# Kernel optimization log

Measured on AMD Instinct MI355X. Metric: run time of the kernel, lower is better.

Reference implementation:

```python
import jax, jax.numpy as jnp
import numpy as np

# Model config (matches init_kwargs)
B, J, D_IN, D_MODEL, NUM_HEADS, NUM_LAYERS = 1024, 24, 64, 512, 8, 6
A = J + 1  # joints + cls token
LN_EPS = 1e-5


def setup_inputs() -> dict:
    key = jax.random.key(0)
    ks = jax.random.split(key, 14)
    s = 0.02  # weight init scale
    return {
        "x": jax.random.normal(ks[0], (B, J, D_IN), dtype=jnp.float32),
        # per-joint input embeddings: Linear(d_in, d_model) x J
        "We": jax.random.normal(ks[1], (J, D_IN, D_MODEL), dtype=jnp.float32) * s,
        "be": jnp.zeros((J, D_MODEL), dtype=jnp.float32),
        "cls_token": jax.random.normal(ks[2], (D_MODEL,), dtype=jnp.float32),
        # per-layer shared key/value projections
        "Wk": jax.random.normal(ks[3], (NUM_LAYERS, D_MODEL, D_MODEL), dtype=jnp.float32) * s,
        "bk": jnp.zeros((NUM_LAYERS, D_MODEL), dtype=jnp.float32),
        "Wv": jax.random.normal(ks[4], (NUM_LAYERS, D_MODEL, D_MODEL), dtype=jnp.float32) * s,
        "bv": jnp.zeros((NUM_LAYERS, D_MODEL), dtype=jnp.float32),
        # per-layer, PER-JOINT query projections (ModuleList of A linears)
        "Wq": jax.random.normal(ks[5], (NUM_LAYERS, A, D_MODEL, D_MODEL), dtype=jnp.float32) * s,
        "bq": jnp.zeros((NUM_LAYERS, A, D_MODEL), dtype=jnp.float32),
        "Wo": jax.random.normal(ks[6], (NUM_LAYERS, D_MODEL, D_MODEL), dtype=jnp.float32) * s,
        "bo": jnp.zeros((NUM_LAYERS, D_MODEL), dtype=jnp.float32),
        "ln_g": jnp.ones((NUM_LAYERS, D_MODEL), dtype=jnp.float32),
        "ln_b": jnp.zeros((NUM_LAYERS, D_MODEL), dtype=jnp.float32),
    }


def _layernorm(y, g, b):
    m = jnp.mean(y, axis=-1, keepdims=True)
    v = jnp.var(y, axis=-1, keepdims=True)  # ddof=0 matches torch LayerNorm
    return (y - m) * jax.lax.rsqrt(v + LN_EPS) * g + b


def reference(x, We, be, cls_token, Wk, bk, Wv, bv, Wq, bq, Wo, bo, ln_g, ln_b):
    b = x.shape[0]
    depth = D_MODEL // NUM_HEADS
    # per-joint input embedding -> (B, J, D)
    tok = jnp.einsum("bjd,jde->bje", x, We) + be
    cls = jnp.broadcast_to(cls_token[None, None, :], (b, 1, D_MODEL))
    h = jnp.concatenate([cls, tok], axis=1)  # (B, A, D); the seq dim of 1 is dropped

    def split(t):  # (B, A, D) -> (B, H, A, depth)
        return t.reshape(b, A, NUM_HEADS, depth).transpose(0, 2, 1, 3)

    for l in range(NUM_LAYERS):
        k = h @ Wk[l] + bk[l]                                  # (B, A, D)
        v = h @ Wv[l] + bv[l]                                  # (B, A, D)
        q = jnp.einsum("bad,ade->bae", h, Wq[l]) + bq[l]        # per-joint query
        qh, kh, vh = split(q), split(k), split(v)
        scores = jnp.einsum("bhqd,bhkd->bhqk", qh, kh) / jnp.sqrt(jnp.float32(depth))
        w = jax.nn.softmax(scores, axis=-1)                    # (B, H, A, A)
        o = jnp.einsum("bhqk,bhkd->bhqd", w, vh)
        o = o.transpose(0, 2, 1, 3).reshape(b, A, D_MODEL)
        o = o @ Wo[l] + bo[l]
        h = _layernorm(h + o, ln_g[l], ln_b[l])
    return h  # (B, A, D) == inputs[:, 0, :, :] in the torch code
```

## Files before the change

### kernel.cpp

```cpp
#include <hip/hip_runtime.h>

typedef unsigned short u16;
typedef unsigned int u32;
typedef short bf16x8 __attribute__((ext_vector_type(8)));
typedef float f32x4 __attribute__((ext_vector_type(4)));

#define AS1 __attribute__((address_space(1)))
#define AS3 __attribute__((address_space(3)))

__device__ __forceinline__ u16 f2b(float f) {
  u32 u = __float_as_uint(f);
  u += 0x7fffu + ((u >> 16) & 1u);
  return (u16)(u >> 16);
}
__device__ __forceinline__ float b2f(u16 s) {
  return __uint_as_float(((u32)s) << 16);
}

__device__ __forceinline__ void gload16(const u16* g, u16* l) {
  __builtin_amdgcn_global_load_lds((const AS1 void*)g, (AS3 void*)l, 16, 0, 0);
}

__global__ __launch_bounds__(256) void prep_kernel(const float* __restrict__ x,
                                                   const float* __restrict__ cls,
                                                   u16* __restrict__ xb,
                                                   u16* __restrict__ hb) {
  if (blockIdx.x < 1536) {
    int i = blockIdx.x * 256 + threadIdx.x;
    float4 v = ((const float4*)x)[i];
    ushort4 u;
    u.x = f2b(v.x); u.y = f2b(v.y); u.z = f2b(v.z); u.w = f2b(v.w);
    ((ushort4*)xb)[i] = u;
  } else {
    int i = (blockIdx.x - 1536) * 256 + threadIdx.x;
    int b = i >> 7;
    int e = (i & 127) << 2;
    float4 v = *(const float4*)(cls + e);
    long off = (long)b * (25 * 512) + e;
    ushort4 u;
    u.x = f2b(v.x); u.y = f2b(v.y); u.z = f2b(v.z); u.w = f2b(v.w);
    *(ushort4*)(hb + off) = u;
  }
}

__device__ __forceinline__ void conv_tile(const float* __restrict__ src,
                                          u16* __restrict__ dst,
                                          int K, int N, int k0, int n0,
                                          void* smem) {
  float (*t)[65] = (float(*)[65])smem;
  for (int i = threadIdx.x; i < 4096; i += 256) {
    int r = i >> 6, c = i & 63;
    t[r][c] = src[(long)(k0 + r) * N + n0 + c];
  }
  __syncthreads();
  for (int i = threadIdx.x; i < 4096; i += 256) {
    int r = i >> 6, c = i & 63;
    dst[(long)(n0 + r) * K + k0 + c] = f2b(t[c][r]);
  }
}

__global__ __launch_bounds__(256) void convT_kernel(const float* __restrict__ src,
                                                    u16* __restrict__ dst,
                                                    int K, int N,
                                                    long src_gstride, long dst_gstride) {
  __shared__ float t[64][65];
  conv_tile(src + (long)blockIdx.z * src_gstride, dst + (long)blockIdx.z * dst_gstride,
            K, N, blockIdx.x * 64, blockIdx.y * 64, t);
}

__global__ __launch_bounds__(256) void convT4_kernel(
    const float* __restrict__ wq, const float* __restrict__ wk,
    const float* __restrict__ wv, const float* __restrict__ wo,
    u16* __restrict__ dq, u16* __restrict__ dk,
    u16* __restrict__ dv, u16* __restrict__ dwo) {
  __shared__ float t[64][65];
  const int z = blockIdx.z;
  const float* src;
  u16* dst;
  if (z < 25)      { src = wq + (long)z * 262144; dst = dq + (long)z * 262144; }
  else if (z == 25){ src = wk; dst = dk; }
  else if (z == 26){ src = wv; dst = dv; }
  else             { src = wo; dst = dwo; }
  conv_tile(src, dst, 512, 512, blockIdx.x * 64, blockIdx.y * 64, t);
}

__device__ __forceinline__ void gemm_core(u16* lds,
    const u16* Ag, long a_stride, const u16* Wg, const float* biasg,
    u16* Cg, long c_stride, int K, int m0, int n0) {
  u16* As = lds;
  u16* Bs = lds + 8192;

  const int tid = threadIdx.x;
  const int lane = tid & 63;
  const int wave = tid >> 6;
  const int wr = wave >> 1, wc = wave & 1;

  const int schunk = lane & 7;
  const u16* ga[4];
  const u16* gb[4];
  int lo[4];
#pragma unroll
  for (int i = 0; i < 4; ++i) {
    const int r = wave * 32 + i * 8 + (lane >> 3);
    const int csw = (schunk ^ (r & 7)) << 3;
    ga[i] = Ag + (long)(m0 + r) * a_stride + csw;
    gb[i] = Wg + (long)(n0 + r) * K + csw;
    lo[i] = (wave * 32 + i * 8) * 64;
  }

  f32x4 acc[4][4];
#pragma unroll
  for (int m = 0; m < 4; ++m)
#pragma unroll
    for (int n = 0; n < 4; ++n) {
      acc[m][n][0] = 0.f; acc[m][n][1] = 0.f;
      acc[m][n][2] = 0.f; acc[m][n][3] = 0.f;
    }

  const int nt = K >> 6;
  for (int t = 0; t < nt; ++t) {
    const int k0 = t << 6;
#pragma unroll
    for (int i = 0; i < 4; ++i) {
      gload16(ga[i] + k0, As + lo[i]);
      gload16(gb[i] + k0, Bs + lo[i]);
    }
    __syncthreads();

#pragma unroll
    for (int kk = 0; kk < 64; kk += 32) {
      const int kb = kk + ((lane >> 4) << 3);
      bf16x8 af[4], bfr[4];
#pragma unroll
      for (int m = 0; m < 4; ++m) {
        const int R = (wr << 6) + (m << 4) + (lane & 15);
        af[m] = *(const bf16x8*)&As[((R << 6) + kb) ^ ((R & 7) << 3)];
      }
#pragma unroll
      for (int n = 0; n < 4; ++n) {
        const int Cc = (wc << 6) + (n << 4) + (lane & 15);
        bfr[n] = *(const bf16x8*)&Bs[((Cc << 6) + kb) ^ ((Cc & 7) << 3)];
      }
#pragma unroll
      for (int m = 0; m < 4; ++m)
#pragma unroll
        for (int n = 0; n < 4; ++n)
          acc[m][n] = __builtin_amdgcn_mfma_f32_16x16x32_bf16(af[m], bfr[n],
                                                              acc[m][n], 0, 0, 0);
    }
    if (t + 1 < nt) __syncthreads();
  }

  const int lcol = lane & 15;
  const int lrow = (lane >> 4) << 2;
#pragma unroll
  for (int n = 0; n < 4; ++n) {
    const int col = n0 + (wc << 6) + (n << 4) + lcol;
    const float bv = biasg[col];
#pragma unroll
    for (int m = 0; m < 4; ++m) {
      const int row = m0 + (wr << 6) + (m << 4) + lrow;
#pragma unroll
      for (int j = 0; j < 4; ++j) {
        const float val = acc[m][n][j] + bv;
        Cg[(long)(row + j) * c_stride + col] = f2b(val);
      }
    }
  }
}

__global__ __launch_bounds__(256) void gemm_plain(
    const u16* __restrict__ Abase, long a_stride, long a_goff,
    const u16* __restrict__ Wbase, long w_gstride,
    const float* __restrict__ biasbase, long bias_gstride,
    u16* __restrict__ Cb, long c_stride, long c_goff, int K) {
  __shared__ u16 lds[16384];
  const int gx = gridDim.x, gy = gridDim.y;
  int lin = blockIdx.x + gx * (blockIdx.y + gy * blockIdx.z);
  const int total = gx * gy * gridDim.z;
  const int chunk = total >> 3;
  lin = (lin & 7) * chunk + (lin >> 3);
  const int g = lin / (gx * gy);
  const int rem = lin % (gx * gy);
  const int mt = rem % gx;
  const int nt = rem / gx;
  gemm_core(lds,
            Abase + (long)g * a_goff, a_stride,
            Wbase + (long)g * w_gstride,
            biasbase + (long)g * bias_gstride,
            Cb + (long)g * c_goff, c_stride, K,
            mt * 128, nt * 128);
}

__global__ __launch_bounds__(256) void gemm_qkv(
    const u16* __restrict__ hb,
    const u16* __restrict__ wqT, const u16* __restrict__ wkT, const u16* __restrict__ wvT,
    const float* __restrict__ bq, const float* __restrict__ bk, const float* __restrict__ bv,
    u16* __restrict__ qb, u16* __restrict__ kb, u16* __restrict__ vb) {
  __shared__ u16 lds[16384];
  const int bid = (blockIdx.x & 7) * 300 + (blockIdx.x >> 3);
  const u16* Ag; long a_str; const u16* Wg; const float* bg; u16* Cg; long c_str;
  int mt, nt;
  if (bid < 800) {
    const int g = bid >> 5, rem = bid & 31;
    mt = rem >> 2; nt = rem & 3;
    Ag = hb + (long)g * 512; a_str = 12800;
    Wg = wqT + (long)g * 262144; bg = bq + (long)g * 512;
    Cg = qb + (long)g * 512; c_str = 12800;
  } else if (bid < 1600) {
    const int rem = bid - 800;
    mt = rem >> 2; nt = rem & 3;
    Ag = hb; a_str = 512; Wg = wkT; bg = bk; Cg = kb; c_str = 512;
  } else {
    const int rem = bid - 1600;
    mt = rem >> 2; nt = rem & 3;
    Ag = hb; a_str = 512; Wg = wvT; bg = bv; Cg = vb; c_str = 512;
  }
  gemm_core(lds, Ag, a_str, Wg, bg, Cg, c_str, 512, mt * 128, nt * 128);
}

__global__ __launch_bounds__(256) void attn_kernel(const u16* __restrict__ q,
                                                   u16* __restrict__ kio,
                                                   const u16* __restrict__ v) {
  __shared__ float ks_[25 * 256];
  __shared__ float vs_[25 * 256];
  const int tid = threadIdx.x;
  const int b = blockIdx.x >> 1;
  const int h0 = blockIdx.x & 1;
  const long base = (long)b * 25 * 512;

  for (int i = tid; i < 800; i += 256) {
    const int j = i >> 5, c = i & 31;
    const long goff = base + (long)j * 512 + h0 * 256 + c * 8;
    uint4 kt = *(const uint4*)(kio + goff);
    uint4 vt = *(const uint4*)(v + goff);
    const u32 ka[4] = {kt.x, kt.y, kt.z, kt.w};
    const u32 va[4] = {vt.x, vt.y, vt.z, vt.w};
    float4 k0f = {b2f((u16)ka[0]), b2f((u16)(ka[0] >> 16)),
                  b2f((u16)ka[1]), b2f((u16)(ka[1] >> 16))};
    float4 k1f = {b2f((u16)ka[2]), b2f((u16)(ka[2] >> 16)),
                  b2f((u16)ka[3]), b2f((u16)(ka[3] >> 16))};
    float4 v0f = {b2f((u16)va[0]), b2f((u16)(va[0] >> 16)),
                  b2f((u16)va[1]), b2f((u16)(va[1] >> 16))};
    float4 v1f = {b2f((u16)va[2]), b2f((u16)(va[2] >> 16)),
                  b2f((u16)va[3]), b2f((u16)(va[3] >> 16))};
    const int off = j * 256 + c * 8;
    *(float4*)&ks_[off]     = k0f;
    *(float4*)&ks_[off + 4] = k1f;
    *(float4*)&vs_[off]     = v0f;
    *(float4*)&vs_[off + 4] = v1f;
  }
  __syncthreads();

  const int w = tid >> 6;
  const int lane = tid & 63;
  const int qi = lane >> 1;
  const int half = lane & 1;
  if (qi < 25) {
    const int h = h0 * 4 + w;
    const int dslice = w * 64 + half * 32;

    const u16* qrow = q + base + (long)qi * 512 + h * 64 + half * 32;
    float buf[32];
#pragma unroll
    for (int c = 0; c < 4; ++c) {
      uint4 t = *(const uint4*)(qrow + c * 8);
      const u32 tt[4] = {t.x, t.y, t.z, t.w};
#pragma unroll
      for (int e = 0; e < 4; ++e) {
        buf[c * 8 + 2 * e]     = b2f((u16)tt[e]);
        buf[c * 8 + 2 * e + 1] = b2f((u16)(tt[e] >> 16));
      }
    }

    float sc[25];
    float mx = -1e30f;
#pragma unroll
    for (int j = 0; j < 25; ++j) {
      const float4* kr = (const float4*)&ks_[j * 256 + dslice];
      float s0 = 0.f, s1 = 0.f;
#pragma unroll
      for (int c4 = 0; c4 < 8; ++c4) {
        float4 kv = kr[c4];
        s0 += buf[4 * c4 + 0] * kv.x + buf[4 * c4 + 1] * kv.y;
        s1 += buf[4 * c4 + 2] * kv.z + buf[4 * c4 + 3] * kv.w;
      }
      float s = s0 + s1;
      s += __shfl_xor(s, 1);
      s *= 0.125f;
      sc[j] = s;
      mx = fmaxf(mx, s);
    }
    float sum = 0.f;
#pragma unroll
    for (int j = 0; j < 25; ++j) {
      sc[j] = __expf(sc[j] - mx);
      sum += sc[j];
    }
    const float inv = 1.f / sum;

#pragma unroll
    for (int d = 0; d < 32; ++d) buf[d] = 0.f;
#pragma unroll
    for (int j = 0; j < 25; ++j) {
      const float wj = sc[j];
      const float4* vr = (const float4*)&vs_[j * 256 + dslice];
#pragma unroll
      for (int c4 = 0; c4 < 8; ++c4) {
        float4 vv = vr[c4];
        buf[4 * c4 + 0] += wj * vv.x;
        buf[4 * c4 + 1] += wj * vv.y;
        buf[4 * c4 + 2] += wj * vv.z;
        buf[4 * c4 + 3] += wj * vv.w;
      }
    }

    u16* orow = kio + base + (long)qi * 512 + h * 64 + half * 32;
#pragma unroll
    for (int c = 0; c < 4; ++c) {
      uint4 t;
      u32 tt[4];
#pragma unroll
      for (int e = 0; e < 4; ++e)
        tt[e] = (u32)f2b(buf[c * 8 + 2 * e] * inv) |
                ((u32)f2b(buf[c * 8 + 2 * e + 1] * inv) << 16);
      t.x = tt[0]; t.y = tt[1]; t.z = tt[2]; t.w = tt[3];
      *(uint4*)(orow + c * 8) = t;
    }
  }
}

__global__ __launch_bounds__(512) void gemm_oln(
    const u16* __restrict__ ao,
    const u16* __restrict__ woT,
    const float* __restrict__ bo,
    u16* __restrict__ hb,
    const float* __restrict__ gam, const float* __restrict__ bet) {
  __shared__ u16 As[4096];
  __shared__ u16 Bs[32768];
  const int tid = threadIdx.x;
  const int lane = tid & 63;
  const int wave = tid >> 6;
  const int mb = (int)(blockIdx.x & 7) * 50 + (int)(blockIdx.x >> 3);
  const int m0 = mb * 64;

  const int sr = tid >> 3;
  const int schunk = ((tid & 7) ^ (sr & 7)) << 3;
  const int aoff = (m0 + sr) * 512 + schunk;
  int boff[8];
#pragma unroll
  for (int i = 0; i < 8; ++i) boff[i] = (i * 64 + sr) * 512 + schunk;
  const int lA = (wave << 3) << 6;
  int lB[8];
#pragma unroll
  for (int i = 0; i < 8; ++i) lB[i] = ((i * 64 + (wave << 3))) << 6;

  f32x4 acc[4][4];
#pragma unroll
  for (int m = 0; m < 4; ++m)
#pragma unroll
    for (int n = 0; n < 4; ++n) {
      acc[m][n][0] = 0.f; acc[m][n][1] = 0.f;
      acc[m][n][2] = 0.f; acc[m][n][3] = 0.f;
    }

  for (int t = 0; t < 8; ++t) {
    const int k0 = t << 6;
    gload16(ao + aoff + k0, As + lA);
#pragma unroll
    for (int i = 0; i < 8; ++i) gload16(woT + boff[i] + k0, Bs + lB[i]);
    __syncthreads();

#pragma unroll
    for (int kk = 0; kk < 64; kk += 32) {
      const int kb = kk + ((lane >> 4) << 3);
      bf16x8 af[4], bfr[4];
#pragma unroll
      for (int m = 0; m < 4; ++m) {
        const int R = (m << 4) + (lane & 15);
        af[m] = *(const bf16x8*)&As[((R << 6) + kb) ^ ((R & 7) << 3)];
      }
#pragma unroll
      for (int n = 0; n < 4; ++n) {
        const int Cc = (wave << 6) + (n << 4) + (lane & 15);
        bfr[n] = *(const bf16x8*)&Bs[((Cc << 6) + kb) ^ ((Cc & 7) << 3)];
      }
#pragma unroll
      for (int m = 0; m < 4; ++m)
#pragma unroll
        for (int n = 0; n < 4; ++n)
          acc[m][n] = __builtin_amdgcn_mfma_f32_16x16x32_bf16(af[m], bfr[n],
                                                              acc[m][n], 0, 0, 0);
    }
    __syncthreads();
  }

  u16* C = Bs;
  {
    const int lcol = lane & 15;
    const int lrow = (lane >> 4) << 2;
#pragma unroll
    for (int n = 0; n < 4; ++n) {
      const int col = (wave << 6) + (n << 4) + lcol;
      const float bv = bo[col];
#pragma unroll
      for (int m = 0; m < 4; ++m) {
#pragma unroll
        for (int j = 0; j < 4; ++j) {
          const int row = (m << 4) + lrow + j;
          C[((row << 9) + col) ^ ((row & 7) << 3)] = f2b(acc[m][n][j] + bv);
        }
      }
    }
  }
  __syncthreads();

  const int ebase = lane << 3;
#pragma unroll
  for (int rr = 0; rr < 8; ++rr) {
    const int row = (rr << 3) + wave;
    uint4 cv = *(const uint4*)&C[((row << 9) + ebase) ^ ((row & 7) << 3)];
    const long grow = (long)(m0 + row) * 512;
    uint4 hv4 = *(const uint4*)(hb + grow + ebase);
    const u32 ha[4] = {hv4.x, hv4.y, hv4.z, hv4.w};
    const u32 oa[4] = {cv.x, cv.y, cv.z, cv.w};
    float y[8];
#pragma unroll
    for (int e = 0; e < 4; ++e) {
      y[2 * e]     = b2f((u16)ha[e])         + b2f((u16)oa[e]);
      y[2 * e + 1] = b2f((u16)(ha[e] >> 16)) + b2f((u16)(oa[e] >> 16));
    }
    float s = 0.f, ss = 0.f;
#pragma unroll
    for (int i = 0; i < 8; ++i) { s += y[i]; ss += y[i] * y[i]; }
#pragma unroll
    for (int off = 32; off > 0; off >>= 1) {
      s += __shfl_down(s, off);
      ss += __shfl_down(ss, off);
    }
    s = __shfl(s, 0);
    ss = __shfl(ss, 0);
    const float mean = s * (1.f / 512.f);
    const float var = ss * (1.f / 512.f) - mean * mean;
    const float rinv = rsqrtf(var + 1e-5f);
    float4 g0 = *(const float4*)(gam + ebase);
    float4 g1 = *(const float4*)(gam + ebase + 4);
    float4 b0 = *(const float4*)(bet + ebase);
    float4 b1 = *(const float4*)(bet + ebase + 4);
    float r[8];
    r[0] = (y[0] - mean) * rinv * g0.x + b0.x;
    r[1] = (y[1] - mean) * rinv * g0.y + b0.y;
    r[2] = (y[2] - mean) * rinv * g0.z + b0.z;
    r[3] = (y[3] - mean) * rinv * g0.w + b0.w;
    r[4] = (y[4] - mean) * rinv * g1.x + b1.x;
    r[5] = (y[5] - mean) * rinv * g1.y + b1.y;
    r[6] = (y[6] - mean) * rinv * g1.z + b1.z;
    r[7] = (y[7] - mean) * rinv * g1.w + b1.w;
    uint4 hv;
    hv.x = (u32)f2b(r[0]) | ((u32)f2b(r[1]) << 16);
    hv.y = (u32)f2b(r[2]) | ((u32)f2b(r[3]) << 16);
    hv.z = (u32)f2b(r[4]) | ((u32)f2b(r[5]) << 16);
    hv.w = (u32)f2b(r[6]) | ((u32)f2b(r[7]) << 16);
    *(uint4*)(hb + grow + ebase) = hv;
  }
}

__global__ __launch_bounds__(256) void ln_kernel(u16* hb,
                                                 const u16* __restrict__ o,
                                                 const float* __restrict__ g,
                                                 const float* __restrict__ bta,
                                                 float* fout) {
  const int lane = threadIdx.x & 63;
  const int wave = threadIdx.x >> 6;
  const long row = (long)blockIdx.x * 4 + wave;
  u16* hr = hb + row * 512;
  const u16* orow = o + row * 512;
  const int base = lane << 3;
  uint4 hv4 = *(const uint4*)(hr + base);
  uint4 ov = *(const uint4*)(orow + base);
  const u32 ha[4] = {hv4.x, hv4.y, hv4.z, hv4.w};
  const u32 oa[4] = {ov.x, ov.y, ov.z, ov.w};
  float y[8];
#pragma unroll
  for (int e = 0; e < 4; ++e) {
    y[2 * e]     = b2f((u16)ha[e])         + b2f((u16)oa[e]);
    y[2 * e + 1] = b2f((u16)(ha[e] >> 16)) + b2f((u16)(oa[e] >> 16));
  }
  float s = 0.f, ss = 0.f;
#pragma unroll
  for (int i = 0; i < 8; ++i) { s += y[i]; ss += y[i] * y[i]; }
#pragma unroll
  for (int off = 32; off > 0; off >>= 1) {
    s += __shfl_down(s, off);
    ss += __shfl_down(ss, off);
  }
  s = __shfl(s, 0);
  ss = __shfl(ss, 0);
  const float mean = s * (1.f / 512.f);
  const float var = ss * (1.f / 512.f) - mean * mean;
  const float rinv = rsqrtf(var + 1e-5f);
  float4 g0 = *(const float4*)(g + base);
  float4 g1 = *(const float4*)(g + base + 4);
  float4 b0 = *(const float4*)(bta + base);
  float4 b1 = *(const float4*)(bta + base + 4);
  float r[8];
  r[0] = (y[0] - mean) * rinv * g0.x + b0.x;
  r[1] = (y[1] - mean) * rinv * g0.y + b0.y;
  r[2] = (y[2] - mean) * rinv * g0.z + b0.z;
  r[3] = (y[3] - mean) * rinv * g0.w + b0.w;
  r[4] = (y[4] - mean) * rinv * g1.x + b1.x;
  r[5] = (y[5] - mean) * rinv * g1.y + b1.y;
  r[6] = (y[6] - mean) * rinv * g1.z + b1.z;
  r[7] = (y[7] - mean) * rinv * g1.w + b1.w;
  uint4 hv;
  hv.x = (u32)f2b(r[0]) | ((u32)f2b(r[1]) << 16);
  hv.y = (u32)f2b(r[2]) | ((u32)f2b(r[3]) << 16);
  hv.z = (u32)f2b(r[4]) | ((u32)f2b(r[5]) << 16);
  hv.w = (u32)f2b(r[6]) | ((u32)f2b(r[7]) << 16);
  *(uint4*)(hr + base) = hv;
  if (fout) {
    float* fr = fout + row * 512 + base;
    float4 w0 = {r[0], r[1], r[2], r[3]};
    float4 w1 = {r[4], r[5], r[6], r[7]};
    *(float4*)(fr) = w0;
    *(float4*)(fr + 4) = w1;
  }
}

extern "C" void kernel_launch(void* const* d_in, const int* in_sizes, int n_in,
                              void* d_out, int out_size, void* d_ws, size_t ws_size,
                              hipStream_t stream) {
  const float* x   = (const float*)d_in[0];
  const float* We  = (const float*)d_in[1];
  const float* be  = (const float*)d_in[2];
  const float* cls = (const float*)d_in[3];
  const float* Wk  = (const float*)d_in[4];
  const float* bk  = (const float*)d_in[5];
  const float* Wv  = (const float*)d_in[6];
  const float* bv  = (const float*)d_in[7];
  const float* Wq  = (const float*)d_in[8];
  const float* bq  = (const float*)d_in[9];
  const float* Wo  = (const float*)d_in[10];
  const float* bo  = (const float*)d_in[11];
  const float* lng = (const float*)d_in[12];
  const float* lnb = (const float*)d_in[13];
  float* out = (float*)d_out;

  char* ws = (char*)d_ws;
  u16* hb = (u16*)ws;
  u16* kb = (u16*)(ws + 26214400);
  u16* vb = (u16*)(ws + 52428800);
  u16* qb = (u16*)(ws + 78643200);
  u16* xb = kb;

  u16* scr = (u16*)d_out;
  u16* weT = scr + 7340032;
  u16* wqT = scr;
  u16* wkT = scr + 6553600;
  u16* wvT = scr + 6815744;
  u16* woT = scr + 7077888;

  prep_kernel<<<2048, 256, 0, stream>>>(x, cls, xb, hb);
  convT_kernel<<<dim3(1, 8, 24), 256, 0, stream>>>(We, weT, 64, 512, 32768, 32768);
  gemm_plain<<<dim3(8, 4, 24), 256, 0, stream>>>(
      xb, 1536, 64, weT, 32768, be, 512, hb + 512, 12800, 512, 64);

  for (int l = 0; l < 6; ++l) {
    convT4_kernel<<<dim3(8, 8, 28), 256, 0, stream>>>(
        Wq + (long)l * 6553600, Wk + (long)l * 262144,
        Wv + (long)l * 262144, Wo + (long)l * 262144,
        wqT, wkT, wvT, woT);
    gemm_qkv<<<2400, 256, 0, stream>>>(
        hb, wqT, wkT, wvT,
        bq + (long)l * 12800, bk + (long)l * 512, bv + (long)l * 512,
        qb, kb, vb);
    attn_kernel<<<2048, 256, 0, stream>>>(qb, kb, vb);
    if (l < 5) {
      gemm_oln<<<400, 512, 0, stream>>>(
          kb, woT, bo + (long)l * 512, hb,
          lng + (long)l * 512, lnb + (long)l * 512);
    } else {
      gemm_plain<<<dim3(200, 4, 1), 256, 0, stream>>>(
          kb, 512, 0, woT, 0, bo + (long)l * 512, 0, qb, 512, 0, 512);
      ln_kernel<<<6400, 256, 0, stream>>>(hb, qb, lng + l * 512, lnb + l * 512, out);
    }
  }
}
```

Baseline: 1.024 ms.

## Use 256x256-tile 8-wave QKV GEMM with pipelined LDS double buffering

Replaces the 128x128-tile QKV projection GEMM with a new kernel that uses 256x256 output tiles, 512 threads (8 waves), and 128 KiB of LDS double-buffered via global_load_lds. Loads for the next K-tile are issued in phases and overlap with MFMA compute, with XOR-swizzled LDS addressing and setprio around the MFMA block. The larger tiles are meant to improve operand reuse and cut global traffic and launch count. In exchange, each block holds a large accumulator set and lots of LDS, which lowers occupancy. With only 600 blocks, the grid may also fill the CUs less evenly.

```diff
diff --git a/kernel.cpp b/kernel.cpp
--- a/kernel.cpp
+++ b/kernel.cpp
@@ -192,31 +192,131 @@
             mt * 128, nt * 128);
 }
 
-__global__ __launch_bounds__(256) void gemm_qkv(
+__global__ __launch_bounds__(512) void gemm_qkv8(
     const u16* __restrict__ hb,
     const u16* __restrict__ wqT, const u16* __restrict__ wkT, const u16* __restrict__ wvT,
     const float* __restrict__ bq, const float* __restrict__ bk, const float* __restrict__ bv,
     u16* __restrict__ qb, u16* __restrict__ kb, u16* __restrict__ vb) {
-  __shared__ u16 lds[16384];
-  const int bid = (blockIdx.x & 7) * 300 + (blockIdx.x >> 3);
-  const u16* Ag; long a_str; const u16* Wg; const float* bg; u16* Cg; long c_str;
-  int mt, nt;
-  if (bid < 800) {
-    const int g = bid >> 5, rem = bid & 31;
-    mt = rem >> 2; nt = rem & 3;
-    Ag = hb + (long)g * 512; a_str = 12800;
-    Wg = wqT + (long)g * 262144; bg = bq + (long)g * 512;
+  __shared__ u16 lds[65536];
+  const int tid = threadIdx.x;
+  const int lane = tid & 63;
+  const int wave = tid >> 6;
+  const int wr = wave >> 2;
+  const int wc = wave & 3;
+
+  const int bid = (blockIdx.x & 7) * 75 + (blockIdx.x >> 3);
+  const u16* Ab; long a_str; const u16* Wt; const float* bias; u16* Cg; long c_str;
+  int m0, n0;
+  if (bid < 200) {
+    const int g = bid >> 3, rem = bid & 7;
+    m0 = (rem >> 1) * 256; n0 = (rem & 1) * 256;
+    Ab = hb + (long)g * 512; a_str = 12800;
+    Wt = wqT + (long)g * 262144; bias = bq + (long)g * 512;
     Cg = qb + (long)g * 512; c_str = 12800;
-  } else if (bid < 1600) {
-    const int rem = bid - 800;
-    mt = rem >> 2; nt = rem & 3;
-    Ag = hb; a_str = 512; Wg = wkT; bg = bk; Cg = kb; c_str = 512;
+  } else if (bid < 400) {
+    const int rem = bid - 200;
+    m0 = (rem >> 1) * 256; n0 = (rem & 1) * 256;
+    Ab = hb; a_str = 512; Wt = wkT; bias = bk; Cg = kb; c_str = 512;
   } else {
-    const int rem = bid - 1600;
-    mt = rem >> 2; nt = rem & 3;
-    Ag = hb; a_str = 512; Wg = wvT; bg = bv; Cg = vb; c_str = 512;
-  }
-  gemm_core(lds, Ag, a_str, Wg, bg, Cg, c_str, 512, mt * 128, nt * 128);
+    const int rem = bid - 400;
+    m0 = (rem >> 1) * 256; n0 = (rem & 1) * 256;
+    Ab = hb; a_str = 512; Wt = wvT; bias = bv; Cg = vb; c_str = 512;
+  }
+
+  const u16* src[4][2];
+  int lo[2];
+#pragma unroll
+  for (int i = 0; i < 2; ++i) {
+    const int r = i * 64 + wave * 8 + (lane >> 3);
+    const int csw = (((lane & 7) ^ (r & 7)) << 3);
+    lo[i] = (i * 64 + wave * 8) * 64;
+#pragma unroll
+    for (int j = 0; j < 2; ++j)
+      src[j][i] = Ab + (long)(m0 + j * 128 + r) * a_str + csw;
+#pragma unroll
+    for (int j = 0; j < 2; ++j)
+      src[2 + j][i] = Wt + (long)(n0 + j * 128 + r) * 512 + csw;
+  }
+
+  f32x4 acc[8][4];
+#pragma unroll
+  for (int m = 0; m < 8; ++m)
+#pragma unroll
+    for (int n = 0; n < 4; ++n) {
+      acc[m][n][0] = 0.f; acc[m][n][1] = 0.f;
+      acc[m][n][2] = 0.f; acc[m][n][3] = 0.f;
+    }
+
+  auto STAGE = [&](int kt, int j) {
+    const int k0 = kt << 6;
+    u16* base = lds + ((j >> 1) << 15) + ((kt & 1) << 14) + ((j & 1) << 13);
+#pragma unroll
+    for (int i = 0; i < 2; ++i)
+      gload16(src[j][i] + k0, base + lo[i]);
+  };
+
+#pragma unroll
+  for (int j = 0; j < 4; ++j) STAGE(0, j);
+
+  const int lq = lane & 15;
+  const int kb0 = (lane >> 4) << 3;
+  const int Rb = (wc & 1) << 6;
+
+  for (int t = 0; t < 8; ++t) {
+    const int d = t & 1;
+    const u16* Al = lds + (d << 14) + (wr << 13);
+    const u16* Bl = lds + 32768 + (d << 14) + ((wc >> 1) << 13);
+
+    __builtin_amdgcn_s_barrier();
+    __builtin_amdgcn_sched_barrier(0);
+
+#pragma unroll
+    for (int ph = 0; ph < 4; ++ph) {
+      if (t < 7) STAGE(t + 1, ph);
+      if (ph == 0) {
+        if (t < 7) asm volatile("s_waitcnt vmcnt(2)" ::: "memory");
+        else       asm volatile("s_waitcnt vmcnt(0)" ::: "memory");
+      }
+      __builtin_amdgcn_s_barrier();
+      __builtin_amdgcn_sched_barrier(0);
+
+      const int mfb = (ph & 1) << 2;
+      const int kb = ((ph >> 1) << 5) + kb0;
+      bf16x8 af[4], bfr[4];
+#pragma unroll
+      for (int q = 0; q < 4; ++q) {
+        const int R = ((mfb + q) << 4) + lq;
+        af[q] = *(const bf16x8*)&Al[((R << 6) + kb) ^ ((R & 7) << 3)];
+      }
+#pragma unroll
+      for (int nf = 0; nf < 4; ++nf) {
+        const int R = Rb + (nf << 4) + lq;
+        bfr[nf] = *(const bf16x8*)&Bl[((R << 6) + kb) ^ ((R & 7) << 3)];
+      }
+      __builtin_amdgcn_s_setprio(1);
+#pragma unroll
+      for (int q = 0; q < 4; ++q)
+#pragma unroll
+        for (int nf = 0; nf < 4; ++nf)
+          acc[mfb + q][nf] = __builtin_amdgcn_mfma_f32_16x16x32_bf16(
+              af[q], bfr[nf], acc[mfb + q][nf], 0, 0, 0);
+      __builtin_amdgcn_s_setprio(0);
+    }
+  }
+
+  const int lrow = (lane >> 4) << 2;
+#pragma unroll
+  for (int nf = 0; nf < 4; ++nf) {
+    const int col = n0 + (wc << 6) + (nf << 4) + lq;
+    const float bv = bias[col];
+#pragma unroll
+    for (int mf = 0; mf < 8; ++mf) {
+      const int row = m0 + (wr << 7) + (mf << 4) + lrow;
+#pragma unroll
+      for (int e = 0; e < 4; ++e)
+        Cg[(long)(row + e) * c_str + col] = f2b(acc[mf][nf][e] + bv);
+    }
+  }
 }
 
 __global__ __launch_bounds__(256) void attn_kernel(const u16* __restrict__ q,
@@ -570,7 +670,7 @@
         Wq + (long)l * 6553600, Wk + (long)l * 262144,
         Wv + (long)l * 262144, Wo + (long)l * 262144,
         wqT, wkT, wvT, woT);
-    gemm_qkv<<<2400, 256, 0, stream>>>(
+    gemm_qkv8<<<600, 512, 0, stream>>>(
         hb, wqT, wkT, wvT,
         bq + (long)l * 12800, bk + (long)l * 512, bv + (long)l * 512,
         qb, kb, vb);
```

Measured after the change: 1.126 ms. +10.0%, slower.

## Double-buffer GEMM LDS tiles, keep attention K/V in bf16 LDS, split prep

Applied to the files above, without the earlier changes.

The GEMM core now uses two LDS buffers, so the global-to-LDS load of the next K tile is issued before computing the current one. This overlaps load latency with MFMA work and leaves one barrier per iteration. The attention kernel stores K/V in LDS as bf16 rather than converting to fp32 at load, which halves LDS use and moves the conversion into the inner loops. The prep kernel is split into separate cast and cls kernels, adding one launch. Doubling GEMM LDS to 64KB per block may lower occupancy.

```diff
diff --git a/kernel.cpp b/kernel.cpp
--- a/kernel.cpp
+++ b/kernel.cpp
@@ -21,26 +21,26 @@
   __builtin_amdgcn_global_load_lds((const AS1 void*)g, (AS3 void*)l, 16, 0, 0);
 }
 
-__global__ __launch_bounds__(256) void prep_kernel(const float* __restrict__ x,
-                                                   const float* __restrict__ cls,
-                                                   u16* __restrict__ xb,
-                                                   u16* __restrict__ hb) {
-  if (blockIdx.x < 1536) {
-    int i = blockIdx.x * 256 + threadIdx.x;
-    float4 v = ((const float4*)x)[i];
-    ushort4 u;
-    u.x = f2b(v.x); u.y = f2b(v.y); u.z = f2b(v.z); u.w = f2b(v.w);
-    ((ushort4*)xb)[i] = u;
-  } else {
-    int i = (blockIdx.x - 1536) * 256 + threadIdx.x;
-    int b = i >> 7;
-    int e = (i & 127) << 2;
-    float4 v = *(const float4*)(cls + e);
-    long off = (long)b * (25 * 512) + e;
-    ushort4 u;
-    u.x = f2b(v.x); u.y = f2b(v.y); u.z = f2b(v.z); u.w = f2b(v.w);
-    *(ushort4*)(hb + off) = u;
-  }
+__global__ __launch_bounds__(256) void cast_kernel(const float* __restrict__ x,
+                                                   u16* __restrict__ xb, int n4) {
+  int i = blockIdx.x * 256 + threadIdx.x;
+  if (i >= n4) return;
+  float4 v = ((const float4*)x)[i];
+  ushort4 u;
+  u.x = f2b(v.x); u.y = f2b(v.y); u.z = f2b(v.z); u.w = f2b(v.w);
+  ((ushort4*)xb)[i] = u;
+}
+
+__global__ __launch_bounds__(256) void cls_kernel(const float* __restrict__ cls,
+                                                  u16* __restrict__ hb) {
+  int i = blockIdx.x * 256 + threadIdx.x;
+  int b = i >> 7;
+  int e = (i & 127) << 2;
+  float4 v = *(const float4*)(cls + e);
+  long off = (long)b * (25 * 512) + e;
+  ushort4 u;
+  u.x = f2b(v.x); u.y = f2b(v.y); u.z = f2b(v.z); u.w = f2b(v.w);
+  *(ushort4*)(hb + off) = u;
 }
 
 __device__ __forceinline__ void conv_tile(const float* __restrict__ src,
@@ -87,8 +87,10 @@
 __device__ __forceinline__ void gemm_core(u16* lds,
     const u16* Ag, long a_stride, const u16* Wg, const float* biasg,
     u16* Cg, long c_stride, int K, int m0, int n0) {
-  u16* As = lds;
-  u16* Bs = lds + 8192;
+  u16* As0 = lds;
+  u16* Bs0 = lds + 8192;
+  u16* As1 = lds + 16384;
+  u16* Bs1 = lds + 24576;
 
   const int tid = threadIdx.x;
   const int lane = tid & 63;
@@ -117,16 +119,14 @@
       acc[m][n][2] = 0.f; acc[m][n][3] = 0.f;
     }
 
-  const int nt = K >> 6;
-  for (int t = 0; t < nt; ++t) {
-    const int k0 = t << 6;
+  auto STAGE = [&](int k0, u16* A, u16* B) {
 #pragma unroll
     for (int i = 0; i < 4; ++i) {
-      gload16(ga[i] + k0, As + lo[i]);
-      gload16(gb[i] + k0, Bs + lo[i]);
-    }
-    __syncthreads();
-
+      gload16(ga[i] + k0, A + lo[i]);
+      gload16(gb[i] + k0, B + lo[i]);
+    }
+  };
+  auto COMPUTE = [&](const u16* A, const u16* B) {
 #pragma unroll
     for (int kk = 0; kk < 64; kk += 32) {
       const int kb = kk + ((lane >> 4) << 3);
@@ -134,12 +134,12 @@
 #pragma unroll
       for (int m = 0; m < 4; ++m) {
         const int R = (wr << 6) + (m << 4) + (lane & 15);
-        af[m] = *(const bf16x8*)&As[((R << 6) + kb) ^ ((R & 7) << 3)];
+        af[m] = *(const bf16x8*)&A[((R << 6) + kb) ^ ((R & 7) << 3)];
       }
 #pragma unroll
       for (int n = 0; n < 4; ++n) {
         const int Cc = (wc << 6) + (n << 4) + (lane & 15);
-        bfr[n] = *(const bf16x8*)&Bs[((Cc << 6) + kb) ^ ((Cc & 7) << 3)];
+        bfr[n] = *(const bf16x8*)&B[((Cc << 6) + kb) ^ ((Cc & 7) << 3)];
       }
 #pragma unroll
       for (int m = 0; m < 4; ++m)
@@ -148,6 +148,20 @@
           acc[m][n] = __builtin_amdgcn_mfma_f32_16x16x32_bf16(af[m], bfr[n],
                                                               acc[m][n], 0, 0, 0);
     }
+  };
+
+  const int nt = K >> 6;
+  STAGE(0, As0, Bs0);
+  __syncthreads();
+  for (int t = 0; t < nt; ++t) {
+    u16* cA = (t & 1) ? As1 : As0;
+    u16* cB = (t & 1) ? Bs1 : Bs0;
+    if (t + 1 < nt) {
+      u16* nA = (t & 1) ? As0 : As1;
+      u16* nB = (t & 1) ? Bs0 : Bs1;
+      STAGE((t + 1) << 6, nA, nB);
+    }
+    COMPUTE(cA, cB);
     if (t + 1 < nt) __syncthreads();
   }
 
@@ -174,7 +188,7 @@
     const u16* __restrict__ Wbase, long w_gstride,
     const float* __restrict__ biasbase, long bias_gstride,
     u16* __restrict__ Cb, long c_stride, long c_goff, int K) {
-  __shared__ u16 lds[16384];
+  __shared__ u16 lds[4 * 8192];
   const int gx = gridDim.x, gy = gridDim.y;
   int lin = blockIdx.x + gx * (blockIdx.y + gy * blockIdx.z);
   const int total = gx * gy * gridDim.z;
@@ -197,7 +211,7 @@
     const u16* __restrict__ wqT, const u16* __restrict__ wkT, const u16* __restrict__ wvT,
     const float* __restrict__ bq, const float* __restrict__ bk, const float* __restrict__ bv,
     u16* __restrict__ qb, u16* __restrict__ kb, u16* __restrict__ vb) {
-  __shared__ u16 lds[16384];
+  __shared__ u16 lds[4 * 8192];
   const int bid = (blockIdx.x & 7) * 300 + (blockIdx.x >> 3);
   const u16* Ag; long a_str; const u16* Wg; const float* bg; u16* Cg; long c_str;
   int mt, nt;
@@ -222,8 +236,8 @@
 __global__ __launch_bounds__(256) void attn_kernel(const u16* __restrict__ q,
                                                    u16* __restrict__ kio,
                                                    const u16* __restrict__ v) {
-  __shared__ float ks_[25 * 256];
-  __shared__ float vs_[25 * 256];
+  __shared__ u16 ks_[25 * 256];
+  __shared__ u16 vs_[25 * 256];
   const int tid = threadIdx.x;
   const int b = blockIdx.x >> 1;
   const int h0 = blockIdx.x & 1;
@@ -232,23 +246,8 @@
   for (int i = tid; i < 800; i += 256) {
     const int j = i >> 5, c = i & 31;
     const long goff = base + (long)j * 512 + h0 * 256 + c * 8;
-    uint4 kt = *(const uint4*)(kio + goff);
-    uint4 vt = *(const uint4*)(v + goff);
-    const u32 ka[4] = {kt.x, kt.y, kt.z, kt.w};
-    const u32 va[4] = {vt.x, vt.y, vt.z, vt.w};
-    float4 k0f = {b2f((u16)ka[0]), b2f((u16)(ka[0] >> 16)),
-                  b2f((u16)ka[1]), b2f((u16)(ka[1] >> 16))};
-    float4 k1f = {b2f((u16)ka[2]), b2f((u16)(ka[2] >> 16)),
-                  b2f((u16)ka[3]), b2f((u16)(ka[3] >> 16))};
-    float4 v0f = {b2f((u16)va[0]), b2f((u16)(va[0] >> 16)),
-                  b2f((u16)va[1]), b2f((u16)(va[1] >> 16))};
-    float4 v1f = {b2f((u16)va[2]), b2f((u16)(va[2] >> 16)),
-                  b2f((u16)va[3]), b2f((u16)(va[3] >> 16))};
-    const int off = j * 256 + c * 8;
-    *(float4*)&ks_[off]     = k0f;
-    *(float4*)&ks_[off + 4] = k1f;
-    *(float4*)&vs_[off]     = v0f;
-    *(float4*)&vs_[off + 4] = v1f;
+    ((uint4*)ks_)[i] = *(const uint4*)(kio + goff);
+    ((uint4*)vs_)[i] = *(const uint4*)(v + goff);
   }
   __syncthreads();
 
@@ -277,15 +276,13 @@
     float mx = -1e30f;
 #pragma unroll
     for (int j = 0; j < 25; ++j) {
-      const float4* kr = (const float4*)&ks_[j * 256 + dslice];
-      float s0 = 0.f, s1 = 0.f;
-#pragma unroll
-      for (int c4 = 0; c4 < 8; ++c4) {
-        float4 kv = kr[c4];
-        s0 += buf[4 * c4 + 0] * kv.x + buf[4 * c4 + 1] * kv.y;
-        s1 += buf[4 * c4 + 2] * kv.z + buf[4 * c4 + 3] * kv.w;
-      }
-      float s = s0 + s1;
+      float s = 0.f;
+      const u16* kr = &ks_[j * 256 + dslice];
+#pragma unroll
+      for (int d = 0; d < 32; d += 2) {
+        u32 t = *(const u32*)(kr + d);
+        s += buf[d] * b2f((u16)t) + buf[d + 1] * b2f((u16)(t >> 16));
+      }
       s += __shfl_xor(s, 1);
       s *= 0.125f;
       sc[j] = s;
@@ -304,14 +301,12 @@
 #pragma unroll
     for (int j = 0; j < 25; ++j) {
       const float wj = sc[j];
-      const float4* vr = (const float4*)&vs_[j * 256 + dslice];
-#pragma unroll
-      for (int c4 = 0; c4 < 8; ++c4) {
-        float4 vv = vr[c4];
-        buf[4 * c4 + 0] += wj * vv.x;
-        buf[4 * c4 + 1] += wj * vv.y;
-        buf[4 * c4 + 2] += wj * vv.z;
-        buf[4 * c4 + 3] += wj * vv.w;
+      const u16* vr = &vs_[j * 256 + dslice];
+#pragma unroll
+      for (int d = 0; d < 32; d += 2) {
+        u32 t = *(const u32*)(vr + d);
+        buf[d]     += wj * b2f((u16)t);
+        buf[d + 1] += wj * b2f((u16)(t >> 16));
       }
     }
 
@@ -560,7 +555,8 @@
   u16* wvT = scr + 6815744;
   u16* woT = scr + 7077888;
 
-  prep_kernel<<<2048, 256, 0, stream>>>(x, cls, xb, hb);
+  cast_kernel<<<1536, 256, 0, stream>>>(x, xb, 393216);
+  cls_kernel<<<512, 256, 0, stream>>>(cls, hb);
   convT_kernel<<<dim3(1, 8, 24), 256, 0, stream>>>(We, weT, 64, 512, 32768, 32768);
   gemm_plain<<<dim3(8, 4, 24), 256, 0, stream>>>(
       xb, 1536, 64, weT, 32768, be, 512, hb + 512, 12800, 512, 64);
```

Result: no change. 1.010 ms (-1.3%).
